# Performance work log

Hardware: AMD Instinct MI355X
Metric: run time of the kernel (lower is better)

## Reference

```python
import jax, jax.numpy as jnp
import numpy as np

B, T, N, H, L, K, E, KSEL = 16, 24, 2000, 64, 2, 2, 3, 2
OUT_LEN = 24
NUM_MAT = 1 + 2 * K  # identity + K powers of each of the 2 supports


def _rw(adj):
    # random-walk matrix D^{-1} A
    d = adj.sum(axis=1)
    return adj / jnp.where(d == 0, 1.0, d)[:, None]


def _dconv(xh, A_q, A_h, W, b):
    # k-hop dual-direction diffusion convolution; xh: [b,n,f]
    feats = [xh]
    for A in (A_q, A_h):
        cur = xh
        for _ in range(K):
            cur = jnp.einsum('nm,bmf->bnf', A, cur)
            feats.append(cur)
    return jnp.concatenate(feats, axis=-1) @ W + b


def _cell(x, h, A_q, A_h, Wg, bg, Wc, bc):
    # DCRNN (diffusion-conv GRU) cell
    xh = jnp.concatenate([x, h], axis=-1)
    ru = jax.nn.sigmoid(_dconv(xh, A_q, A_h, Wg, bg))
    r, u = jnp.split(ru, 2, axis=-1)
    c = jnp.tanh(_dconv(jnp.concatenate([x, r * h], axis=-1), A_q, A_h, Wc, bc))
    return u * h + (1.0 - u) * c


def setup_inputs() -> dict:
    key = jax.random.key(0)
    ks = jax.random.split(key, 24)
    s = 0.02
    nrm = lambda k, shp: (jax.random.normal(k, shp) * s).astype(jnp.float32)
    adj = (jax.random.uniform(ks[0], (N, N)) * (jax.random.uniform(ks[1], (N, N)) < 0.05)).astype(jnp.float32)
    x_enc = jax.random.normal(ks[2], (B, T, N, 1), dtype=jnp.float32)
    x_enc = x_enc * (jax.random.uniform(ks[3], (B, T, N, 1)) < 0.7)
    x_dec = jax.random.normal(ks[4], (B, OUT_LEN, N, 1), dtype=jnp.float32)

    def cell_p(k, fin):
        k1, k2 = jax.random.split(k)
        fcat = NUM_MAT * (fin + H)
        return (nrm(k1, (fcat, 2 * H)), jnp.zeros(2 * H, jnp.float32),
                nrm(k2, (fcat, H)), jnp.zeros(H, jnp.float32))

    e0 = cell_p(ks[5], 1)
    e1 = cell_p(ks[6], H)
    d0 = cell_p(ks[7], 1)
    d1 = cell_p(ks[8], H)
    return dict(
        adj=adj, x_enc=x_enc, x_dec=x_dec,
        gate_w1=nrm(ks[9], (T, H)), gate_b1=jnp.zeros(H, jnp.float32),
        gate_w2=nrm(ks[10], (H, E)), gate_b2=jnp.zeros(E, jnp.float32),
        ew_mean=nrm(ks[11], (T, T)), eb_mean=jnp.zeros(T, jnp.float32),
        ew_wmean=nrm(ks[12], (T, T)), eb_wmean=jnp.zeros(T, jnp.float32),
        ew_diff=nrm(ks[13], (T, T)), eb_diff=jnp.zeros(T, jnp.float32),
        enc0_Wg=e0[0], enc0_bg=e0[1], enc0_Wc=e0[2], enc0_bc=e0[3],
        enc1_Wg=e1[0], enc1_bg=e1[1], enc1_Wc=e1[2], enc1_bc=e1[3],
        dec0_Wg=d0[0], dec0_bg=d0[1], dec0_Wc=d0[2], dec0_bc=d0[3],
        dec1_Wg=d1[0], dec1_bg=d1[1], dec1_Wc=d1[2], dec1_bc=d1[3],
        fc_w=nrm(ks[14], (H, 1)), fc_b=jnp.zeros(1, jnp.float32),
        epoch=10,
    )


def reference(adj, x_enc, x_dec, gate_w1, gate_b1, gate_w2, gate_b2,
              ew_mean, eb_mean, ew_wmean, eb_wmean, ew_diff, eb_diff,
              enc0_Wg, enc0_bg, enc0_Wc, enc0_bc, enc1_Wg, enc1_bg, enc1_Wc, enc1_bc,
              dec0_Wg, dec0_bg, dec0_Wc, dec0_bc, dec1_Wg, dec1_bg, dec1_Wc, dec1_bc,
              fc_w, fc_b, epoch):
    A_q = _rw(adj)
    A_h = _rw(adj.T)

    # ---- DataPreparation: MoE-gated graph imputation ----
    x = jnp.transpose(x_enc[..., 0], (0, 2, 1))  # [b, n, t]
    g = jax.nn.relu(x @ gate_w1 + gate_b1)
    logits = g @ gate_w2 + gate_b2               # [b, n, E]
    top, idx = jax.lax.top_k(logits, KSEL)
    w = jax.nn.softmax(top, axis=-1)
    gate = (w[..., None] * jax.nn.one_hot(idx, E, dtype=x.dtype)).sum(axis=-2)  # [b,n,E]

    adj_ns = adj * (1.0 - jnp.eye(N, dtype=adj.dtype))
    deg_bin = (adj_ns > 0).astype(x.dtype)
    A_mean = deg_bin / jnp.maximum(deg_bin.sum(axis=1, keepdims=True), 1.0)
    rs = adj_ns.sum(axis=1, keepdims=True)
    A_wmean = adj_ns / jnp.where(rs == 0, 1.0, rs)
    A_diff = _rw(adj_ns)

    outs = [jnp.einsum('nm,bmt->bnt', A_agg, x) @ W + b
            for A_agg, W, b in ((A_mean, ew_mean, eb_mean),
                                (A_wmean, ew_wmean, eb_wmean),
                                (A_diff, ew_diff, eb_diff))]
    combined = (gate[..., None] * jnp.stack(outs, axis=2)).sum(axis=2)  # [b,n,t]
    x = jnp.where(x == 0, combined, x)
    x_imp = jnp.transpose(x, (0, 2, 1))[..., None]  # [b,t,n,1]

    # ---- Encoder: scan over time, 2 DCRNN layers ----
    enc_params = ((enc0_Wg, enc0_bg, enc0_Wc, enc0_bc),
                  (enc1_Wg, enc1_bg, enc1_Wc, enc1_bc))

    def enc_step(h, xt):
        inp = xt
        hs = []
        for l in range(L):
            nh = _cell(inp, h[l], A_q, A_h, *enc_params[l])
            inp = nh
            hs.append(nh)
        return jnp.stack(hs), None

    h0 = jnp.zeros((L, B, N, H), x_imp.dtype)
    hT, _ = jax.lax.scan(enc_step, h0, jnp.transpose(x_imp, (1, 0, 2, 3)))

    dec_params = ((dec0_Wg, dec0_bg, dec0_Wc, dec0_bc),
                  (dec1_Wg, dec1_bg, dec1_Wc, dec1_bc))

    def dec_step(carry, _):
        inp, h = carry
        hs = []
        for l in range(L):
            nh = _cell(inp, h[l], A_q, A_h, *dec_params[l])
            inp = nh
            hs.append(nh)
        out = nh @ fc_w + fc_b  # [b,n,1]
        return (out, jnp.stack(hs)), out

    _, outs_t = jax.lax.scan(dec_step, (x_imp[:, -1], hT), None, length=OUT_LEN)
    return jnp.transpose(outs_t, (1, 0, 2, 3))  # [b, out_len, n, 1]
```

## Files before the change

### kernel.cpp

```cpp
#include <hip/hip_runtime.h>

#define NROW 2000
#define NB   16
#define NT   24
#define NH   64
#define NM   (NROW*NB)
#define HOPLDS (NROW*64)
#define ENT_CAP 262144

typedef _Float16 h16;
typedef __attribute__((ext_vector_type(2))) _Float16 h16x2;
typedef __attribute__((ext_vector_type(8))) _Float16 h16x8;
typedef __attribute__((ext_vector_type(4))) float    f32x4;

__device__ __forceinline__ h16x2 bc_h2(unsigned int u){ union{unsigned int u; h16x2 h;} c; c.u=u; return c.h; }

__global__ __launch_bounds__(256) void k_count(const float* adj, int* cnt_q, int* cnt_h, int* cnt_ns,
    float* rsum_q, float* rsum_h, float* rsum_ns, int* deg_ns){
  int wid = (blockIdx.x*256 + threadIdx.x)>>6;
  int lane = threadIdx.x & 63;
  int kind = wid / NROW, n = wid - kind*NROW;
  int cnt = 0; float sum = 0.f;
  for (int c = lane; c < NROW; c += 64){
    float v = (kind==1) ? adj[(size_t)c*NROW + n] : adj[(size_t)n*NROW + c];
    if (kind==2 && c==n) v = 0.f;
    cnt += (v != 0.f); sum += v;
  }
  for (int off=32; off; off>>=1){ cnt += __shfl_down(cnt,off); sum += __shfl_down(sum,off); }
  if (lane==0){
    int pc = (cnt+7)&~7;
    if (kind==0){ cnt_q[n]=pc; rsum_q[n]=sum; }
    else if (kind==1){ cnt_h[n]=pc; rsum_h[n]=sum; }
    else { cnt_ns[n]=pc; rsum_ns[n]=sum; deg_ns[n]=cnt; }
  }
}

__global__ __launch_bounds__(1024) void k_scan(const int* cq, const int* ch, const int* cn,
    int* rq, int* rh, int* rn){
  __shared__ int s0[2048], s1[2048], s2[2048];
  int t = threadIdx.x;
  for (int a=0;a<2;a++){ int i=t+a*1024; s0[i]= i<NROW?cq[i]:0; s1[i]= i<NROW?ch[i]:0; s2[i]= i<NROW?cn[i]:0; }
  __syncthreads();
  for (int off=1; off<2048; off<<=1){
    int v0[2],v1[2],v2[2];
    for (int a=0;a<2;a++){ int i=t+a*1024; v0[a]= i>=off? s0[i-off]:0; v1[a]= i>=off? s1[i-off]:0; v2[a]= i>=off? s2[i-off]:0; }
    __syncthreads();
    for (int a=0;a<2;a++){ int i=t+a*1024; s0[i]+=v0[a]; s1[i]+=v1[a]; s2[i]+=v2[a]; }
    __syncthreads();
  }
  for (int a=0;a<2;a++){ int i=t+a*1024; if (i<=NROW){ rq[i]= i? s0[i-1]:0; rh[i]= i? s1[i-1]:0; rn[i]= i? s2[i-1]:0; } }
}

__global__ __launch_bounds__(1024) void k_sort(const int* c0, const int* c1, const int* c2,
                                               int* o0, int* o1, int* o2){
  const int* cnt = blockIdx.x==0 ? c0 : blockIdx.x==1 ? c1 : c2;
  int* order     = blockIdx.x==0 ? o0 : blockIdx.x==1 ? o1 : o2;
  __shared__ int hist[256];
  __shared__ int offs[256];
  int tid = threadIdx.x;
  if (tid < 256) hist[tid] = 0;
  __syncthreads();
  for (int r = tid; r < NROW; r += 1024){
    int b = cnt[r] >> 4; if (b > 255) b = 255;
    atomicAdd(&hist[b], 1);
  }
  __syncthreads();
  if (tid == 0){ int s = 0; for (int i=0;i<256;i++){ offs[i] = s; s += hist[i]; } }
  __syncthreads();
  for (int r = tid; r < NROW; r += 1024){
    int b = cnt[r] >> 4; if (b > 255) b = 255;
    int p = atomicAdd(&offs[b], 1);
    order[p] = r;
  }
}

__device__ __forceinline__ uint2 mk_ent(int c, float a){
  h16 h = (h16)a;
  unsigned short us = __builtin_bit_cast(unsigned short, h);
  return make_uint2((unsigned int)(c*64), (unsigned int)us * 0x10001u);
}

__global__ __launch_bounds__(256) void k_fill(const float* adj, const int* rptr_q, const int* rptr_h, const int* rptr_ns,
    const float* rsum_q, const float* rsum_h, const float* rsum_ns, const int* deg_ns,
    uint2* ent_q, uint2* ent_h, uint2* ent_m, uint2* ent_w){
  int wid = (blockIdx.x*256 + threadIdx.x)>>6;
  int lane = threadIdx.x & 63;
  int kind = wid / NROW, n = wid - kind*NROW;
  const int* rp = (kind==0)?rptr_q:(kind==1)?rptr_h:rptr_ns;
  int p = rp[n], pend = rp[n+1];
  float inv, invm = 0.f;
  if (kind==0){ float d = rsum_q[n]; inv = d!=0.f?1.f/d:0.f; }
  else if (kind==1){ float d = rsum_h[n]; inv = d!=0.f?1.f/d:0.f; }
  else { float d = rsum_ns[n]; inv = d!=0.f?1.f/d:0.f; int dg = deg_ns[n]; invm = 1.f/(float)(dg>1?dg:1); }
  int base = 0;
  unsigned long long below = (1ull<<lane)-1ull;
  for (int c0=0; c0<NROW; c0+=64){
    int c = c0+lane; float v = 0.f;
    if (c < NROW){ v = (kind==1)? adj[(size_t)c*NROW+n] : adj[(size_t)n*NROW+c]; if (kind==2 && c==n) v = 0.f; }
    unsigned long long m = __ballot(v != 0.f);
    if (v != 0.f){
      int pos = p + base + __popcll(m & below);
      if (kind==2){ ent_w[pos] = mk_ent(c, v*inv); ent_m[pos] = mk_ent(c, invm); }
      else if (kind==0) ent_q[pos] = mk_ent(c, v*inv);
      else              ent_h[pos] = mk_ent(c, v*inv);
    }
    base += __popcll(m);
  }
  for (int i = p+base+lane; i < pend; i += 64){
    uint2 z = make_uint2(0u,0u);
    if (kind==2){ ent_w[i]=z; ent_m[i]=z; } else if (kind==0) ent_q[i]=z; else ent_h[i]=z;
  }
}

struct HopJob { const h16* X; const int* rptr; const uint2* ent; const int* order; h16* out; };

__device__ __forceinline__ void proc2(const char* xs, int cl, uint4 p, h16x2 ha[4]){
  union{f32x4 v; h16x2 h[4];} ca, cb;
  ca.v = *(const f32x4*)(xs + p.x + cl);
  cb.v = *(const f32x4*)(xs + p.z + cl);
  h16x2 va = bc_h2(p.y), vb = bc_h2(p.w);
  ha[0] = ca.h[0]*va + ha[0];
  ha[1] = ca.h[1]*va + ha[1];
  ha[2] = ca.h[2]*va + ha[2];
  ha[3] = ca.h[3]*va + ha[3];
  ha[0] = cb.h[0]*vb + ha[0];
  ha[1] = cb.h[1]*vb + ha[1];
  ha[2] = cb.h[2]*vb + ha[2];
  ha[3] = cb.h[3]*vb + ha[3];
}

__global__ __launch_bounds__(1024) void k_hop(HopJob j0, HopJob j1, HopJob j2, HopJob j3,
                                              int coltiles, int rsplit, int C){
  extern __shared__ char xs[];
  int per = coltiles*rsplit;
  int bid = blockIdx.x;
  int jb = bid/per, rem = bid - jb*per;
  int ct = rem/rsplit, rs = rem - ct*rsplit;
  HopJob j = (jb==0)?j0:(jb==1)?j1:(jb==2)?j2:j3;
  int c0 = ct*32;
  int tid = threadIdx.x;
  {
    int r0 = tid>>2, so = tid&3;
    const char* src = (const char*)j.X + (size_t)2*(c0 + so*8);
    char* dst = xs + so*16;
    for (int r = r0; r < NROW; r += 256)
      *(f32x4*)(dst + r*64) = *(const f32x4*)(src + (size_t)2*r*C);
  }
  __syncthreads();
  int lane = tid&63, wv = tid>>6;
  int g = lane>>2;
  int cl = (lane&3)*16;
  for (int k = wv; ; k += 16){
    int gu = rs + k*rsplit;
    if (gu >= 125) break;
    int n = j.order[gu*16 + g];
    {
      int p0 = j.rptr[n], cnt = j.rptr[n+1]-p0;
      const uint4* ep4 = (const uint4*)(j.ent + p0);
      float f[8] = {0.f,0.f,0.f,0.f,0.f,0.f,0.f,0.f};
      if (cnt > 0){
        uint4 cur[8];
        #pragma unroll
        for (int u2=0;u2<8;u2++) cur[u2] = ep4[u2];
        int i = 0;
        for (; i+16 <= cnt; i += 16){
          uint4 nx[8];
          int b = (i>>1)+8;
          #pragma unroll
          for (int u2=0;u2<8;u2++) nx[u2] = ep4[b+u2];
          h16x2 ha[4] = {{(_Float16)0.f,(_Float16)0.f},{(_Float16)0.f,(_Float16)0.f},
                         {(_Float16)0.f,(_Float16)0.f},{(_Float16)0.f,(_Float16)0.f}};
          #pragma unroll
          for (int u2=0;u2<8;u2++) proc2(xs, cl, cur[u2], ha);
          f[0] += (float)ha[0][0]; f[1] += (float)ha[0][1];
          f[2] += (float)ha[1][0]; f[3] += (float)ha[1][1];
          f[4] += (float)ha[2][0]; f[5] += (float)ha[2][1];
          f[6] += (float)ha[3][0]; f[7] += (float)ha[3][1];
          #pragma unroll
          for (int u2=0;u2<8;u2++) cur[u2] = nx[u2];
        }
        if (i < cnt){
          h16x2 ha[4] = {{(_Float16)0.f,(_Float16)0.f},{(_Float16)0.f,(_Float16)0.f},
                         {(_Float16)0.f,(_Float16)0.f},{(_Float16)0.f,(_Float16)0.f}};
          proc2(xs, cl, cur[0], ha);
          proc2(xs, cl, cur[1], ha);
          proc2(xs, cl, cur[2], ha);
          proc2(xs, cl, cur[3], ha);
          f[0] += (float)ha[0][0]; f[1] += (float)ha[0][1];
          f[2] += (float)ha[1][0]; f[3] += (float)ha[1][1];
          f[4] += (float)ha[2][0]; f[5] += (float)ha[2][1];
          f[6] += (float)ha[3][0]; f[7] += (float)ha[3][1];
        }
      }
      alignas(16) h16 ov[8];
      #pragma unroll
      for (int k2=0;k2<8;k2++) ov[k2] = (h16)f[k2];
      *(uint4*)((char*)j.out + (size_t)2*((size_t)n*C + c0) + cl) = *(const uint4*)ov;
    }
  }
}

__global__ void k_evinit(const float* rq, const float* rh, float* eq, float* eh){
  int n = blockIdx.x*256+threadIdx.x; if (n>=NROW) return;
  eq[n] = rq[n]!=0.f?1.f:0.f; eh[n] = rh[n]!=0.f?1.f:0.f;
}

__global__ __launch_bounds__(256) void k_matvec(const int* rptr, const uint2* ent, const float* vin, float* vout){
  int wid = (blockIdx.x*256+threadIdx.x)>>6; int lane = threadIdx.x&63;
  if (wid >= NROW) return;
  int p0 = rptr[wid], p1 = rptr[wid+1];
  float s = 0.f;
  for (int i=p0+lane; i<p1; i+=64){
    uint2 e = ent[i];
    int idx = (int)(e.x>>6);
    h16 hv = __builtin_bit_cast(h16, (unsigned short)(e.y & 0xffffu));
    s += (float)hv * vin[idx];
  }
  for (int off=32; off; off>>=1) s += __shfl_down(s,off);
  if (lane==0) vout[wid] = s;
}

__global__ void k_bias2(const float* W, const float* fcb, const float* e1, const float* e2,
                        const float* e3, const float* e4, float* dst, int O){
  int idx = blockIdx.x*256+threadIdx.x; if (idx >= NROW*O) return;
  int n = idx/O, o = idx - n*O;
  float v = W[o] + e1[n]*W[(size_t)65*O+o] + e2[n]*W[(size_t)130*O+o]
                 + e3[n]*W[(size_t)195*O+o] + e4[n]*W[(size_t)260*O+o];
  dst[idx] = fcb[0]*v;
}

__global__ void k_wpack(const float* W, const float* fcw, h16* dst, int O, int nch, int mode){
  int idx = blockIdx.x*256+threadIdx.x; if (idx >= nch*O*32) return;
  int k = idx&31; int o = (idx>>5)%O; int ch = idx/(O*32);
  float v = 0.f;
  if (mode==0){
    if (ch < 10){ int m = ch>>1, j = (ch&1)*32 + k; v = W[(size_t)(m*65+1+j)*O + o]; }
    else if (k < 5) v = W[(size_t)(k*65)*O + o];
  } else if (mode==1){
    int m = ch>>2, j = (ch&3)*32 + k; v = W[(size_t)(m*128+j)*O + o];
  } else {
    if (ch < 10){ int m = ch>>1, j = (ch&1)*32 + k; v = fcw[j]*W[(size_t)(m*65)*O + o]; }
    else { int c2 = ch-10; int m = c2>>1, j = (c2&1)*32 + k; v = W[(size_t)(m*65+1+j)*O + o]; }
  }
  dst[(size_t)(ch*O + o)*32 + k] = (h16)v;
}

__global__ __launch_bounds__(256) void k_impute_gate(const float* x_enc, const float* gw1, const float* gb1,
// ... 181 lines not shown
{
  const float* adj   = (const float*)d_in[0];
  const float* x_enc = (const float*)d_in[1];
  const float* gw1   = (const float*)d_in[3];
  const float* gb1   = (const float*)d_in[4];
  const float* gw2   = (const float*)d_in[5];
  const float* gb2   = (const float*)d_in[6];
  const float* ewm   = (const float*)d_in[7];
  const float* ebm   = (const float*)d_in[8];
  const float* eww   = (const float*)d_in[9];
  const float* ebw   = (const float*)d_in[10];
  const float* ewd   = (const float*)d_in[11];
  const float* ebd   = (const float*)d_in[12];
  const float* Wg[4] = {(const float*)d_in[13],(const float*)d_in[17],(const float*)d_in[21],(const float*)d_in[25]};
  const float* bg[4] = {(const float*)d_in[14],(const float*)d_in[18],(const float*)d_in[22],(const float*)d_in[26]};
  const float* Wc[4] = {(const float*)d_in[15],(const float*)d_in[19],(const float*)d_in[23],(const float*)d_in[27]};
  const float* bc[4] = {(const float*)d_in[16],(const float*)d_in[20],(const float*)d_in[24],(const float*)d_in[28]};
  const float* fcw   = (const float*)d_in[29];
  const float* fcb   = (const float*)d_in[30];
  float* outp = (float*)d_out;
  (void)in_sizes; (void)n_in; (void)out_size; (void)ws_size;

  char* base = (char*)d_ws;
  size_t off = 0;
  auto alloc = [&](size_t sz)->char*{ char* p = base + off; off += (sz + 255) & ~(size_t)255; return p; };

  uint2* ent_q = (uint2*)alloc(ENT_CAP*8);
  uint2* ent_h = (uint2*)alloc(ENT_CAP*8);
  uint2* ent_m = (uint2*)alloc(ENT_CAP*8);
  uint2* ent_w = (uint2*)alloc(ENT_CAP*8);
  int* rptr_q = (int*)alloc(2001*4);
  int* rptr_h = (int*)alloc(2001*4);
  int* rptr_n = (int*)alloc(2001*4);
  int* cnt_q = (int*)alloc(NROW*4);
  int* cnt_h = (int*)alloc(NROW*4);
  int* cnt_n = (int*)alloc(NROW*4);
  int* ord_q = (int*)alloc(NROW*4);
  int* ord_h = (int*)alloc(NROW*4);
  int* ord_n = (int*)alloc(NROW*4);
  float* rsum_q = (float*)alloc(NROW*4);
  float* rsum_h = (float*)alloc(NROW*4);
  float* rsum_n = (float*)alloc(NROW*4);
  int* deg_n = (int*)alloc(NROW*4);
  float* evq1 = (float*)alloc(NROW*4);
  float* evq2 = (float*)alloc(NROW*4);
  float* evh1 = (float*)alloc(NROW*4);
  float* evh2 = (float*)alloc(NROW*4);
  float* gate3 = (float*)alloc((size_t)NM*3*4);
  h16* xpack = (h16*)alloc((size_t)NT*NM*8*2);
  h16* wp_e0g = (h16*)alloc(11*128*64); h16* wp_e0c = (h16*)alloc(11*64*64);
  h16* wp_e1g = (h16*)alloc(20*128*64); h16* wp_e1c = (h16*)alloc(20*64*64);
  h16* wp_d0gE= (h16*)alloc(11*128*64); h16* wp_d0cE= (h16*)alloc(11*64*64);
  h16* wp_d0gW= (h16*)alloc(20*128*64); h16* wp_d0cW= (h16*)alloc(20*64*64);
  h16* wp_d1g = (h16*)alloc(20*128*64); h16* wp_d1c = (h16*)alloc(20*64*64);
  float* bias2g = (float*)alloc((size_t)NROW*128*4);
  float* bias2c = (float*)alloc((size_t)NROW*64*4);
  const size_t SEG = (size_t)NM*NH*2;
  h16* h0 = (h16*)alloc(SEG);
  h16* h1 = (h16*)alloc(SEG);
  float* ub = (float*)alloc((size_t)NM*NH*4);
  h16* rh = (h16*)alloc(SEG);
  h16* zb = (h16*)alloc(SEG);
  h16* H0Q1=(h16*)alloc(SEG); h16* H0Q2=(h16*)alloc(SEG); h16* H0H1=(h16*)alloc(SEG); h16* H0H2=(h16*)alloc(SEG);
  h16* H1Q1=(h16*)alloc(SEG); h16* H1Q2=(h16*)alloc(SEG); h16* H1H1=(h16*)alloc(SEG); h16* H1H2=(h16*)alloc(SEG);
  h16* RHQ1=(h16*)alloc(SEG); h16* RHQ2=(h16*)alloc(SEG); h16* RHH1=(h16*)alloc(SEG); h16* RHH2=(h16*)alloc(SEG);
  h16* xT   = RHQ1;  h16* Zm = RHQ2;  h16* Zw = RHH1;  h16* ximp = RHH2;
  h16* xq1  = H1Q1;  h16* xq2 = H1Q2; h16* xh1 = H1H1; h16* xh2 = H1H2;

  hipFuncSetAttribute(reinterpret_cast<const void*>(k_hop),
                      hipFuncAttributeMaxDynamicSharedMemorySize, HOPLDS);

  hipMemsetAsync(zb, 0, SEG, stream);
  hipMemsetAsync(h0, 0, SEG, stream);
  hipMemsetAsync(h1, 0, SEG, stream);

  k_count<<<1500,256,0,stream>>>(adj, cnt_q, cnt_h, cnt_n, rsum_q, rsum_h, rsum_n, deg_n);
  k_sort<<<3,1024,0,stream>>>(cnt_q, cnt_h, cnt_n, ord_q, ord_h, ord_n);
  k_scan<<<1,1024,0,stream>>>(cnt_q, cnt_h, cnt_n, rptr_q, rptr_h, rptr_n);
  k_fill<<<1500,256,0,stream>>>(adj, rptr_q, rptr_h, rptr_n, rsum_q, rsum_h, rsum_n, deg_n,
                                ent_q, ent_h, ent_m, ent_w);
  k_evinit<<<8,256,0,stream>>>(rsum_q, rsum_h, evq1, evh1);
  k_matvec<<<500,256,0,stream>>>(rptr_q, ent_q, evq1, evq2);
  k_matvec<<<500,256,0,stream>>>(rptr_h, ent_h, evh1, evh2);
  k_bias2<<<1000,256,0,stream>>>(Wg[2], fcb, evq1, evq2, evh1, evh2, bias2g, 128);
  k_bias2<<<500,256,0,stream>>>(Wc[2], fcb, evq1, evq2, evh1, evh2, bias2c, 64);
  auto wpk = [&](const float* W, h16* dst, int O, int nch, int mode){
    k_wpack<<<(nch*O*32+255)/256,256,0,stream>>>(W, fcw, dst, O, nch, mode);
  };
  wpk(Wg[0], wp_e0g, 128, 11, 0); wpk(Wc[0], wp_e0c, 64, 11, 0);
  wpk(Wg[1], wp_e1g, 128, 20, 1); wpk(Wc[1], wp_e1c, 64, 20, 1);
  wpk(Wg[2], wp_d0gE,128, 11, 0); wpk(Wc[2], wp_d0cE,64, 11, 0);
  wpk(Wg[2], wp_d0gW,128, 20, 2); wpk(Wc[2], wp_d0cW,64, 20, 2);
  wpk(Wg[3], wp_d1g, 128, 20, 1); wpk(Wc[3], wp_d1c, 64, 20, 1);

  k_impute_gate<<<125,256,0,stream>>>(x_enc, gw1, gb1, gw2, gb2, gate3, xT);

  auto hop = [&](HopJob a, HopJob b, HopJob c, HopJob d, int nj, int C, int rsplit){
    int ct = C/32;
    k_hop<<<nj*ct*rsplit, 1024, HOPLDS, stream>>>(a,b,c,d, ct, rsplit, C);
  };
  HopJob JA{xT, rptr_n, ent_m, ord_n, Zm}, JB{xT, rptr_n, ent_w, ord_n, Zw};
  hop(JA, JB, JA, JB, 2, NB*NT, 10);
  k_impute_combine<<<125,256,0,stream>>>(x_enc, Zm, Zw, gate3, ewm, ebm, eww, ebw, ewd, ebd, ximp);
  HopJob X1{ximp, rptr_q, ent_q, ord_q, xq1}, X2{ximp, rptr_h, ent_h, ord_h, xh1};
  hop(X1, X2, X1, X2, 2, NB*NT, 10);
  HopJob X3{xq1, rptr_q, ent_q, ord_q, xq2}, X4{xh1, rptr_h, ent_h, ord_h, xh2};
  hop(X3, X4, X3, X4, 2, NB*NT, 10);
  k_xpack8<<<(NT*NM+255)/256,256,0,stream>>>(ximp, xq1, xq2, xh1, xh2, xpack);

  h16* HSEG0[5] = {h0, H0Q1, H0Q2, H0H1, H0H2};
  h16* HSEG1[5] = {h1, H1Q1, H1Q2, H1H1, H1H2};
  h16* RSEG[5]  = {rh, RHQ1, RHQ2, RHH1, RHH2};
  h16* ZSEG[5]  = {zb, zb, zb, zb, zb};

  auto shapeA = [&](GArgs& A, h16* const* seg, const h16* xpk){
    for (int m=0;m<5;m++) for (int s=0;s<2;s++){ int ch=2*m+s; A.src[ch]=seg[m]; A.rstrideB[ch]=NH*2; A.coffB[ch]=s*64; }
    A.src[10]=xpk; A.rstrideB[10]=16; A.coffB[10]=0; A.nchunks=11; A.xchunk=10;
  };
  auto shapeB = [&](GArgs& A, h16* const* sa, h16* const* sb){
    for (int m=0;m<5;m++) for (int s=0;s<4;s++){ int ch=4*m+s;
      A.src[ch] = (s<2)? sa[m] : sb[m]; A.rstrideB[ch]=NH*2; A.coffB[ch]=(s&1)*64; }
    A.nchunks=20; A.xchunk=-1;
  };
  auto shapeC = [&](GArgs& A, h16* const* segH, h16* const* segX){
    for (int m=0;m<5;m++) for (int s=0;s<2;s++){
      int ch=2*m+s; A.src[ch]=segX[m]; A.rstrideB[ch]=NH*2; A.coffB[ch]=s*64;
      int c2=10+2*m+s; A.src[c2]=segH[m]; A.rstrideB[c2]=NH*2; A.coffB[c2]=s*64; }
    A.nchunks=20; A.xchunk=-1;
  };
  auto common = [&](GArgs& A, const h16* wp, const float* bias, const h16* hb, const float* b2, int t){
    A.wpack=wp; A.bias=bias; A.hbuf=hb; A.rhbuf=rh; A.ubuf=ub; A.hout=(h16*)hb;
    A.bias2=b2; A.fcw=fcw; A.fcb=fcb; A.dout=outp; A.tstep=t;
  };

  for (int phase=0; phase<2; phase++){
    int ig = phase? 2 : 0;
    const h16* wpg0E = phase? wp_d0gE : wp_e0g;
    const h16* wpc0E = phase? wp_d0cE : wp_e0c;
    const h16* wpg1  = phase? wp_d1g  : wp_e1g;
    const h16* wpc1  = phase? wp_d1c  : wp_e1c;
    for (int t=0;t<NT;t++){
      bool wprime = (phase==1 && t>0);
      if (wprime){
        HopJob a{h1, rptr_q, ent_q, ord_q, H1Q1}, b{h1, rptr_h, ent_h, ord_h, H1H1};
        hop(a,b,a,b, 2, NB*NH, 4);
        HopJob c{H1Q1, rptr_q, ent_q, ord_q, H1Q2}, d{H1H1, rptr_h, ent_h, ord_h, H1H2};
        hop(c,d,c,d, 2, NB*NH, 4);
      }
      {
        GArgs A{};
        if (wprime) shapeC(A, HSEG0, HSEG1);
        else shapeA(A, (phase==0 && t==0)? ZSEG : HSEG0, xpack + (size_t)((phase==0)? t : 23)*NM*8);
        common(A, wprime? wp_d0gW : wpg0E, bg[ig], h0, bias2g, t);
        if (wprime) k_g<128,1,1,0><<<500,256,0,stream>>>(A);
        else        k_g<128,1,0,0><<<500,256,0,stream>>>(A);
      }
      if (wprime){
        HopJob a{rh, rptr_q, ent_q, ord_q, RHQ1}, b{rh, rptr_h, ent_h, ord_h, RHH1};
        hop(a,b,a,b, 2, NB*NH, 4);
        HopJob c{RHQ1, rptr_q, ent_q, ord_q, RHQ2}, d{RHH1, rptr_h, ent_h, ord_h, RHH2};
        hop(c,d,c,d, 2, NB*NH, 4);
      } else {
        HopJob a{rh, rptr_q, ent_q, ord_q, RHQ1}, b{rh, rptr_h, ent_h, ord_h, RHH1};
        HopJob c{h1, rptr_q, ent_q, ord_q, H1Q1}, d{h1, rptr_h, ent_h, ord_h, H1H1};
        hop(a,b,c,d, 4, NB*NH, 2);
        HopJob a2{RHQ1, rptr_q, ent_q, ord_q, RHQ2}, b2{RHH1, rptr_h, ent_h, ord_h, RHH2};
        HopJob c2{H1Q1, rptr_q, ent_q, ord_q, H1Q2}, d2{H1H1, rptr_h, ent_h, ord_h, H1H2};
        hop(a2,b2,c2,d2, 4, NB*NH, 2);
      }
      {
        GArgs A{};
        if (wprime) shapeC(A, RSEG, HSEG1);
        else shapeA(A, RSEG, xpack + (size_t)((phase==0)? t : 23)*NM*8);
        common(A, wprime? wp_d0cW : wpc0E, bc[ig], h0, bias2c, t);
        if (wprime) k_g<64,0,1,0><<<500,256,0,stream>>>(A);
        else        k_g<64,0,0,0><<<500,256,0,stream>>>(A);
      }
      {
        HopJob a{h0, rptr_q, ent_q, ord_q, H0Q1}, b{h0, rptr_h, ent_h, ord_h, H0H1};
        hop(a,b,a,b, 2, NB*NH, 4);
        HopJob c{H0Q1, rptr_q, ent_q, ord_q, H0Q2}, d{H0H1, rptr_h, ent_h, ord_h, H0H2};
        hop(c,d,c,d, 2, NB*NH, 4);
      }
      {
        GArgs A{};
        shapeB(A, HSEG0, HSEG1);
        common(A, wpg1, bg[ig+1], h1, nullptr, t);
        k_g<128,1,0,0><<<500,256,0,stream>>>(A);
      }
      {
        HopJob a{rh, rptr_q, ent_q, ord_q, RHQ1}, b{rh, rptr_h, ent_h, ord_h, RHH1};
        hop(a,b,a,b, 2, NB*NH, 4);
        HopJob c{RHQ1, rptr_q, ent_q, ord_q, RHQ2}, d{RHH1, rptr_h, ent_h, ord_h, RHH2};
        hop(c,d,c,d, 2, NB*NH, 4);
      }
      {
        GArgs A{};
        shapeB(A, HSEG0, RSEG);
        common(A, wpc1, bc[ig+1], h1, nullptr, t);
        if (phase) k_g<64,0,0,1><<<500,256,0,stream>>>(A);
        else       k_g<64,0,0,0><<<500,256,0,stream>>>(A);
      }
    }
  }
}
```

Measured before the change: 13.03 ms.

## Split sparse hop into two row-halves with 64-column LDS tiles

Each CSR row is split into two segments by column (<1000 and >=1000), padded separately, with a new rmid array. The hop kernel now stages only 1000 rows of X at a time but 64 columns wide (128B per row) in LDS. It accumulates the first half, restages the second half, and accumulates again, with each wave processing 4 output rows held in registers. The aim is to halve the number of column tiles per job (so less redundant entry reading across tiles) and widen each gather. The cost is a second sync-and-stage pass, extra padding, and a shorter unroll per chunk. Rsplit values are raised to keep enough blocks in flight.

```diff
diff --git a/kernel.cpp b/kernel.cpp
--- a/kernel.cpp
+++ b/kernel.cpp
@@ -5,7 +5,7 @@
 #define NT   24
 #define NH   64
 #define NM   (NROW*NB)
-#define HOPLDS (NROW*64)
+#define HOPLDS (1000*128)
 #define ENT_CAP 262144
 
 typedef _Float16 h16;
@@ -15,23 +15,26 @@
 
 __device__ __forceinline__ h16x2 bc_h2(unsigned int u){ union{unsigned int u; h16x2 h;} c; c.u=u; return c.h; }
 
-__global__ __launch_bounds__(256) void k_count(const float* adj, int* cnt_q, int* cnt_h, int* cnt_ns,
-    float* rsum_q, float* rsum_h, float* rsum_ns, int* deg_ns){
+__global__ __launch_bounds__(256) void k_count(const float* adj, int* cnt_q, int* cnt_h, int* cnt_n,
+    int* pA_q, int* pA_h, int* pA_n,
+    float* rsum_q, float* rsum_h, float* rsum_n, int* deg_n){
   int wid = (blockIdx.x*256 + threadIdx.x)>>6;
   int lane = threadIdx.x & 63;
   int kind = wid / NROW, n = wid - kind*NROW;
-  int cnt = 0; float sum = 0.f;
+  int cA = 0, cB = 0; float sum = 0.f;
   for (int c = lane; c < NROW; c += 64){
     float v = (kind==1) ? adj[(size_t)c*NROW + n] : adj[(size_t)n*NROW + c];
     if (kind==2 && c==n) v = 0.f;
-    cnt += (v != 0.f); sum += v;
-  }
-  for (int off=32; off; off>>=1){ cnt += __shfl_down(cnt,off); sum += __shfl_down(sum,off); }
+    if (v != 0.f){ if (c < 1000) cA++; else cB++; sum += v; }
+  }
+  for (int off=32; off; off>>=1){
+    cA += __shfl_down(cA,off); cB += __shfl_down(cB,off); sum += __shfl_down(sum,off);
+  }
   if (lane==0){
-    int pc = (cnt+7)&~7;
-    if (kind==0){ cnt_q[n]=pc; rsum_q[n]=sum; }
-    else if (kind==1){ cnt_h[n]=pc; rsum_h[n]=sum; }
-    else { cnt_ns[n]=pc; rsum_ns[n]=sum; deg_ns[n]=cnt; }
+    int pa = (cA+7)&~7, pb = (cB+7)&~7;
+    if (kind==0){ cnt_q[n]=pa+pb; pA_q[n]=pa; rsum_q[n]=sum; }
+    else if (kind==1){ cnt_h[n]=pa+pb; pA_h[n]=pa; rsum_h[n]=sum; }
+    else { cnt_n[n]=pa+pb; pA_n[n]=pa; rsum_n[n]=sum; deg_n[n]=cA+cB; }
   }
 }
 
@@ -51,6 +54,16 @@
   for (int a=0;a<2;a++){ int i=t+a*1024; if (i<=NROW){ rq[i]= i? s0[i-1]:0; rh[i]= i? s1[i-1]:0; rn[i]= i? s2[i-1]:0; } }
 }
 
+__global__ void k_rmid(const int* rq, const int* rh, const int* rn,
+                       const int* paq, const int* pah, const int* pan,
+                       int* mq, int* mh, int* mn){
+  int i = blockIdx.x*256+threadIdx.x; if (i >= 3*NROW) return;
+  int kind = i/NROW, n = i - kind*NROW;
+  if (kind==0) mq[n] = rq[n]+paq[n];
+  else if (kind==1) mh[n] = rh[n]+pah[n];
+  else mn[n] = rn[n]+pan[n];
+}
+
 __global__ __launch_bounds__(1024) void k_sort(const int* c0, const int* c1, const int* c2,
                                                int* o0, int* o1, int* o2){
   const int* cnt = blockIdx.x==0 ? c0 : blockIdx.x==1 ? c1 : c2;
@@ -74,45 +87,55 @@
   }
 }
 
-__device__ __forceinline__ uint2 mk_ent(int c, float a){
+__device__ __forceinline__ uint2 mk_ent(unsigned int off_bytes, float a){
   h16 h = (h16)a;
   unsigned short us = __builtin_bit_cast(unsigned short, h);
-  return make_uint2((unsigned int)(c*64), (unsigned int)us * 0x10001u);
-}
-
-__global__ __launch_bounds__(256) void k_fill(const float* adj, const int* rptr_q, const int* rptr_h, const int* rptr_ns,
-    const float* rsum_q, const float* rsum_h, const float* rsum_ns, const int* deg_ns,
+  return make_uint2(off_bytes, (unsigned int)us * 0x10001u);
+}
+
+__global__ __launch_bounds__(256) void k_fill(const float* adj,
+    const int* rptr_q, const int* rptr_h, const int* rptr_n,
+    const int* rmid_q, const int* rmid_h, const int* rmid_n,
+    const float* rsum_q, const float* rsum_h, const float* rsum_n, const int* deg_n,
     uint2* ent_q, uint2* ent_h, uint2* ent_m, uint2* ent_w){
   int wid = (blockIdx.x*256 + threadIdx.x)>>6;
   int lane = threadIdx.x & 63;
   int kind = wid / NROW, n = wid - kind*NROW;
-  const int* rp = (kind==0)?rptr_q:(kind==1)?rptr_h:rptr_ns;
-  int p = rp[n], pend = rp[n+1];
+  const int* rp = (kind==0)?rptr_q:(kind==1)?rptr_h:rptr_n;
+  const int* rm = (kind==0)?rmid_q:(kind==1)?rmid_h:rmid_n;
+  int p = rp[n], pend = rp[n+1], mid = rm[n];
   float inv, invm = 0.f;
   if (kind==0){ float d = rsum_q[n]; inv = d!=0.f?1.f/d:0.f; }
   else if (kind==1){ float d = rsum_h[n]; inv = d!=0.f?1.f/d:0.f; }
-  else { float d = rsum_ns[n]; inv = d!=0.f?1.f/d:0.f; int dg = deg_ns[n]; invm = 1.f/(float)(dg>1?dg:1); }
-  int base = 0;
+  else { float d = rsum_n[n]; inv = d!=0.f?1.f/d:0.f; int dg = deg_n[n]; invm = 1.f/(float)(dg>1?dg:1); }
+  int baseA = 0, baseB = 0;
   unsigned long long below = (1ull<<lane)-1ull;
   for (int c0=0; c0<NROW; c0+=64){
     int c = c0+lane; float v = 0.f;
     if (c < NROW){ v = (kind==1)? adj[(size_t)c*NROW+n] : adj[(size_t)n*NROW+c]; if (kind==2 && c==n) v = 0.f; }
-    unsigned long long m = __ballot(v != 0.f);
-    if (v != 0.f){
-      int pos = p + base + __popcll(m & below);
-      if (kind==2){ ent_w[pos] = mk_ent(c, v*inv); ent_m[pos] = mk_ent(c, invm); }
-      else if (kind==0) ent_q[pos] = mk_ent(c, v*inv);
-      else              ent_h[pos] = mk_ent(c, v*inv);
-    }
-    base += __popcll(m);
-  }
-  for (int i = p+base+lane; i < pend; i += 64){
-    uint2 z = make_uint2(0u,0u);
+    bool nz = (v != 0.f);
+    unsigned long long mA = __ballot(nz && c < 1000);
+    unsigned long long mB = __ballot(nz && c >= 1000);
+    if (nz){
+      int pos; unsigned int off;
+      if (c < 1000){ pos = p + baseA + __popcll(mA & below); off = (unsigned int)(c*128); }
+      else         { pos = mid + baseB + __popcll(mB & below); off = (unsigned int)((c-1000)*128); }
+      if (kind==2){ ent_w[pos] = mk_ent(off, v*inv); ent_m[pos] = mk_ent(off, invm); }
+      else if (kind==0) ent_q[pos] = mk_ent(off, v*inv);
+      else              ent_h[pos] = mk_ent(off, v*inv);
+    }
+    baseA += __popcll(mA); baseB += __popcll(mB);
+  }
+  uint2 z = make_uint2(0u,0u);
+  for (int i = p+baseA+lane; i < mid; i += 64){
     if (kind==2){ ent_w[i]=z; ent_m[i]=z; } else if (kind==0) ent_q[i]=z; else ent_h[i]=z;
   }
-}
-
-struct HopJob { const h16* X; const int* rptr; const uint2* ent; const int* order; h16* out; };
+  for (int i = mid+baseB+lane; i < pend; i += 64){
+    if (kind==2){ ent_w[i]=z; ent_m[i]=z; } else if (kind==0) ent_q[i]=z; else ent_h[i]=z;
+  }
+}
+
+struct HopJob { const h16* X; const int* rptr; const int* rmid; const uint2* ent; const int* order; h16* out; };
 
 __device__ __forceinline__ void proc2(const char* xs, int cl, uint4 p, h16x2 ha[4]){
   union{f32x4 v; h16x2 h[4];} ca, cb;
@@ -129,6 +152,34 @@
   ha[3] = cb.h[3]*vb + ha[3];
 }
 
+__device__ __forceinline__ void accum_row(const char* xs, int cl, const uint2* ent,
+                                          int p0, int p1, float f[8]){
+  int cnt = p1 - p0;
+  if (cnt <= 0) return;
+  const uint4* ep4 = (const uint4*)(ent + p0);
+  uint4 cur[4];
+  #pragma unroll
+  for (int u=0;u<4;u++) cur[u] = ep4[u];
+  for (int i=0; i<cnt; i+=8){
+    uint4 nx[4];
+    if (i+8 < cnt){
+      int b = (i>>1)+4;
+      #pragma unroll
+      for (int u=0;u<4;u++) nx[u] = ep4[b+u];
+    }
+    h16x2 ha[4] = {{(_Float16)0.f,(_Float16)0.f},{(_Float16)0.f,(_Float16)0.f},
+                   {(_Float16)0.f,(_Float16)0.f},{(_Float16)0.f,(_Float16)0.f}};
+    #pragma unroll
+    for (int u=0;u<4;u++) proc2(xs, cl, cur[u], ha);
+    f[0] += (float)ha[0][0]; f[1] += (float)ha[0][1];
+    f[2] += (float)ha[1][0]; f[3] += (float)ha[1][1];
+    f[4] += (float)ha[2][0]; f[5] += (float)ha[2][1];
+    f[6] += (float)ha[3][0]; f[7] += (float)ha[3][1];
+    #pragma unroll
+    for (int u=0;u<4;u++) cur[u] = nx[u];
+  }
+}
+
 __global__ __launch_bounds__(1024) void k_hop(HopJob j0, HopJob j1, HopJob j2, HopJob j3,
                                               int coltiles, int rsplit, int C){
   extern __shared__ char xs[];
@@ -137,64 +188,54 @@
   int jb = bid/per, rem = bid - jb*per;
   int ct = rem/rsplit, rs = rem - ct*rsplit;
   HopJob j = (jb==0)?j0:(jb==1)?j1:(jb==2)?j2:j3;
-  int c0 = ct*32;
+  int c0 = ct*64;
   int tid = threadIdx.x;
+  int lane = tid&63, wv = tid>>6;
+  int g = lane>>3;
+  int cl = (lane&7)*16;
+
+  int nslot[4];
+  #pragma unroll
+  for (int u=0;u<4;u++){
+    int gu = rs + (wv + u*16)*rsplit;
+    nslot[u] = (gu < 250) ? j.order[gu*8 + g] : -1;
+  }
+  float f[4][8];
+  #pragma unroll
+  for (int u=0;u<4;u++)
+    #pragma unroll
+    for (int k2=0;k2<8;k2++) f[u][k2] = 0.f;
+
   {
-    int r0 = tid>>2, so = tid&3;
+    int r0 = tid>>3, so = tid&7;
     const char* src = (const char*)j.X + (size_t)2*(c0 + so*8);
     char* dst = xs + so*16;
-    for (int r = r0; r < NROW; r += 256)
-      *(f32x4*)(dst + r*64) = *(const f32x4*)(src + (size_t)2*r*C);
+    for (int r = r0; r < 1000; r += 128)
+      *(f32x4*)(dst + r*128) = *(const f32x4*)(src + (size_t)2*(size_t)r*C);
   }
   __syncthreads();
-  int lane = tid&63, wv = tid>>6;
-  int g = lane>>2;
-  int cl = (lane&3)*16;
-  for (int k = wv; ; k += 16){
-    int gu = rs + k*rsplit;
-    if (gu >= 125) break;
-    int n = j.order[gu*16 + g];
-    {
-      int p0 = j.rptr[n], cnt = j.rptr[n+1]-p0;
-      const uint4* ep4 = (const uint4*)(j.ent + p0);
-      float f[8] = {0.f,0.f,0.f,0.f,0.f,0.f,0.f,0.f};
-      if (cnt > 0){
-        uint4 cur[8];
-        #pragma unroll
-        for (int u2=0;u2<8;u2++) cur[u2] = ep4[u2];
-        int i = 0;
-        for (; i+16 <= cnt; i += 16){
-          uint4 nx[8];
-          int b = (i>>1)+8;
-          #pragma unroll
-          for (int u2=0;u2<8;u2++) nx[u2] = ep4[b+u2];
-          h16x2 ha[4] = {{(_Float16)0.f,(_Float16)0.f},{(_Float16)0.f,(_Float16)0.f},
-                         {(_Float16)0.f,(_Float16)0.f},{(_Float16)0.f,(_Float16)0.f}};
-          #pragma unroll
-          for (int u2=0;u2<8;u2++) proc2(xs, cl, cur[u2], ha);
-          f[0] += (float)ha[0][0]; f[1] += (float)ha[0][1];
-          f[2] += (float)ha[1][0]; f[3] += (float)ha[1][1];
-          f[4] += (float)ha[2][0]; f[5] += (float)ha[2][1];
-          f[6] += (float)ha[3][0]; f[7] += (float)ha[3][1];
-          #pragma unroll
-          for (int u2=0;u2<8;u2++) cur[u2] = nx[u2];
-        }
-        if (i < cnt){
-          h16x2 ha[4] = {{(_Float16)0.f,(_Float16)0.f},{(_Float16)0.f,(_Float16)0.f},
-                         {(_Float16)0.f,(_Float16)0.f},{(_Float16)0.f,(_Float16)0.f}};
-          proc2(xs, cl, cur[0], ha);
-          proc2(xs, cl, cur[1], ha);
-          proc2(xs, cl, cur[2], ha);
-          proc2(xs, cl, cur[3], ha);
-          f[0] += (float)ha[0][0]; f[1] += (float)ha[0][1];
-          f[2] += (float)ha[1][0]; f[3] += (float)ha[1][1];
-          f[4] += (float)ha[2][0]; f[5] += (float)ha[2][1];
-          f[6] += (float)ha[3][0]; f[7] += (float)ha[3][1];
-        }
-      }
+  #pragma unroll
+  for (int u=0;u<4;u++){
+    int n = nslot[u];
+    if (n >= 0) accum_row(xs, cl, j.ent, j.rptr[n], j.rmid[n], f[u]);
+  }
+  __syncthreads();
+  {
+    int r0 = tid>>3, so = tid&7;
+    const char* src = (const char*)j.X + (size_t)2*((size_t)1000*C + c0 + so*8);
+    char* dst = xs + so*16;
+    for (int r = r0; r < 1000; r += 128)
+      *(f32x4*)(dst + r*128) = *(const f32x4*)(src + (size_t)2*(size_t)r*C);
+  }
+  __syncthreads();
+  #pragma unroll
+  for (int u=0;u<4;u++){
+    int n = nslot[u];
+    if (n >= 0){
+      accum_row(xs, cl, j.ent, j.rmid[n], j.rptr[n+1], f[u]);
       alignas(16) h16 ov[8];
       #pragma unroll
-      for (int k2=0;k2<8;k2++) ov[k2] = (h16)f[k2];
+      for (int k2=0;k2<8;k2++) ov[k2] = (h16)f[u][k2];
       *(uint4*)((char*)j.out + (size_t)2*((size_t)n*C + c0) + cl) = *(const uint4*)ov;
     }
   }
@@ -205,14 +246,15 @@
   eq[n] = rq[n]!=0.f?1.f:0.f; eh[n] = rh[n]!=0.f?1.f:0.f;
 }
 
-__global__ __launch_bounds__(256) void k_matvec(const int* rptr, const uint2* ent, const float* vin, float* vout){
+__global__ __launch_bounds__(256) void k_matvec(const int* rptr, const int* rmid, const uint2* ent,
+                                                const float* vin, float* vout){
   int wid = (blockIdx.x*256+threadIdx.x)>>6; int lane = threadIdx.x&63;
   if (wid >= NROW) return;
-  int p0 = rptr[wid], p1 = rptr[wid+1];
+  int p0 = rptr[wid], p1 = rptr[wid+1], mid = rmid[wid];
   float s = 0.f;
   for (int i=p0+lane; i<p1; i+=64){
     uint2 e = ent[i];
-    int idx = (int)(e.x>>6);
+    int idx = (int)(e.x>>7) + ((i >= mid) ? 1000 : 0);
     h16 hv = __builtin_bit_cast(h16, (unsigned short)(e.y & 0xffffu));
     s += (float)hv * vin[idx];
   }
@@ -460,9 +502,15 @@
   int* rptr_q = (int*)alloc(2001*4);
   int* rptr_h = (int*)alloc(2001*4);
   int* rptr_n = (int*)alloc(2001*4);
+  int* rmid_q = (int*)alloc(NROW*4);
+  int* rmid_h = (int*)alloc(NROW*4);
+  int* rmid_n = (int*)alloc(NROW*4);
   int* cnt_q = (int*)alloc(NROW*4);
   int* cnt_h = (int*)alloc(NROW*4);
   int* cnt_n = (int*)alloc(NROW*4);
+  int* pA_q = (int*)alloc(NROW*4);
+  int* pA_h = (int*)alloc(NROW*4);
+  int* pA_n = (int*)alloc(NROW*4);
   int* ord_q = (int*)alloc(NROW*4);
   int* ord_h = (int*)alloc(NROW*4);
   int* ord_n = (int*)alloc(NROW*4);
@@ -502,14 +550,17 @@
   hipMemsetAsync(h0, 0, SEG, stream);
   hipMemsetAsync(h1, 0, SEG, stream);
 
-  k_count<<<1500,256,0,stream>>>(adj, cnt_q, cnt_h, cnt_n, rsum_q, rsum_h, rsum_n, deg_n);
+  k_count<<<1500,256,0,stream>>>(adj, cnt_q, cnt_h, cnt_n, pA_q, pA_h, pA_n,
+                                 rsum_q, rsum_h, rsum_n, deg_n);
   k_sort<<<3,1024,0,stream>>>(cnt_q, cnt_h, cnt_n, ord_q, ord_h, ord_n);
   k_scan<<<1,1024,0,stream>>>(cnt_q, cnt_h, cnt_n, rptr_q, rptr_h, rptr_n);
-  k_fill<<<1500,256,0,stream>>>(adj, rptr_q, rptr_h, rptr_n, rsum_q, rsum_h, rsum_n, deg_n,
+  k_rmid<<<24,256,0,stream>>>(rptr_q, rptr_h, rptr_n, pA_q, pA_h, pA_n, rmid_q, rmid_h, rmid_n);
+  k_fill<<<1500,256,0,stream>>>(adj, rptr_q, rptr_h, rptr_n, rmid_q, rmid_h, rmid_n,
+                                rsum_q, rsum_h, rsum_n, deg_n,
                                 ent_q, ent_h, ent_m, ent_w);
   k_evinit<<<8,256,0,stream>>>(rsum_q, rsum_h, evq1, evh1);
-  k_matvec<<<500,256,0,stream>>>(rptr_q, ent_q, evq1, evq2);
-  k_matvec<<<500,256,0,stream>>>(rptr_h, ent_h, evh1, evh2);
+  k_matvec<<<500,256,0,stream>>>(rptr_q, rmid_q, ent_q, evq1, evq2);
+  k_matvec<<<500,256,0,stream>>>(rptr_h, rmid_h, ent_h, evh1, evh2);
   k_bias2<<<1000,256,0,stream>>>(Wg[2], fcb, evq1, evq2, evh1, evh2, bias2g, 128);
   k_bias2<<<500,256,0,stream>>>(Wc[2], fcb, evq1, evq2, evh1, evh2, bias2c, 64);
   auto wpk = [&](const float* W, h16* dst, int O, int nch, int mode){
@@ -524,16 +575,16 @@
   k_impute_gate<<<125,256,0,stream>>>(x_enc, gw1, gb1, gw2, gb2, gate3, xT);
 
   auto hop = [&](HopJob a, HopJob b, HopJob c, HopJob d, int nj, int C, int rsplit){
-    int ct = C/32;
+    int ct = C/64;
     k_hop<<<nj*ct*rsplit, 1024, HOPLDS, stream>>>(a,b,c,d, ct, rsplit, C);
   };
-  HopJob JA{xT, rptr_n, ent_m, ord_n, Zm}, JB{xT, rptr_n, ent_w, ord_n, Zw};
-  hop(JA, JB, JA, JB, 2, NB*NT, 10);
+  HopJob JA{xT, rptr_n, rmid_n, ent_m, ord_n, Zm}, JB{xT, rptr_n, rmid_n, ent_w, ord_n, Zw};
+  hop(JA, JB, JA, JB, 2, NB*NT, 16);
   k_impute_combine<<<125,256,0,stream>>>(x_enc, Zm, Zw, gate3, ewm, ebm, eww, ebw, ewd, ebd, ximp);
-  HopJob X1{ximp, rptr_q, ent_q, ord_q, xq1}, X2{ximp, rptr_h, ent_h, ord_h, xh1};
-  hop(X1, X2, X1, X2, 2, NB*NT, 10);
-  HopJob X3{xq1, rptr_q, ent_q, ord_q, xq2}, X4{xh1, rptr_h, ent_h, ord_h, xh2};
-  hop(X3, X4, X3, X4, 2, NB*NT, 10);
+  HopJob X1{ximp, rptr_q, rmid_q, ent_q, ord_q, xq1}, X2{ximp, rptr_h, rmid_h, ent_h, ord_h, xh1};
+  hop(X1, X2, X1, X2, 2, NB*NT, 16);
+  HopJob X3{xq1, rptr_q, rmid_q, ent_q, ord_q, xq2}, X4{xh1, rptr_h, rmid_h, ent_h, ord_h, xh2};
+  hop(X3, X4, X3, X4, 2, NB*NT, 16);
   k_xpack8<<<(NT*NM+255)/256,256,0,stream>>>(ximp, xq1, xq2, xh1, xh2, xpack);
 
   h16* HSEG0[5] = {h0, H0Q1, H0Q2, H0H1, H0H2};
@@ -570,10 +621,10 @@
     for (int t=0;t<NT;t++){
       bool wprime = (phase==1 && t>0);
       if (wprime){
-        HopJob a{h1, rptr_q, ent_q, ord_q, H1Q1}, b{h1, rptr_h, ent_h, ord_h, H1H1};
-        hop(a,b,a,b, 2, NB*NH, 4);
-        HopJob c{H1Q1, rptr_q, ent_q, ord_q, H1Q2}, d{H1H1, rptr_h, ent_h, ord_h, H1H2};
-        hop(c,d,c,d, 2, NB*NH, 4);
+        HopJob a{h1, rptr_q, rmid_q, ent_q, ord_q, H1Q1}, b{h1, rptr_h, rmid_h, ent_h, ord_h, H1H1};
+        hop(a,b,a,b, 2, NB*NH, 8);
+        HopJob c{H1Q1, rptr_q, rmid_q, ent_q, ord_q, H1Q2}, d{H1H1, rptr_h, rmid_h, ent_h, ord_h, H1H2};
+        hop(c,d,c,d, 2, NB*NH, 8);
       }
       {
         GArgs A{};
@@ -584,17 +635,17 @@
         else        k_g<128,1,0,0><<<500,256,0,stream>>>(A);
       }
       if (wprime){
-        HopJob a{rh, rptr_q, ent_q, ord_q, RHQ1}, b{rh, rptr_h, ent_h, ord_h, RHH1};
-        hop(a,b,a,b, 2, NB*NH, 4);
-        HopJob c{RHQ1, rptr_q, ent_q, ord_q, RHQ2}, d{RHH1, rptr_h, ent_h, ord_h, RHH2};
-        hop(c,d,c,d, 2, NB*NH, 4);
+        HopJob a{rh, rptr_q, rmid_q, ent_q, ord_q, RHQ1}, b{rh, rptr_h, rmid_h, ent_h, ord_h, RHH1};
+        hop(a,b,a,b, 2, NB*NH, 8);
+        HopJob c{RHQ1, rptr_q, rmid_q, ent_q, ord_q, RHQ2}, d{RHH1, rptr_h, rmid_h, ent_h, ord_h, RHH2};
+        hop(c,d,c,d, 2, NB*NH, 8);
       } else {
-        HopJob a{rh, rptr_q, ent_q, ord_q, RHQ1}, b{rh, rptr_h, ent_h, ord_h, RHH1};
-        HopJob c{h1, rptr_q, ent_q, ord_q, H1Q1}, d{h1, rptr_h, ent_h, ord_h, H1H1};
-        hop(a,b,c,d, 4, NB*NH, 2);
-        HopJob a2{RHQ1, rptr_q, ent_q, ord_q, RHQ2}, b2{RHH1, rptr_h, ent_h, ord_h, RHH2};
-        HopJob c2{H1Q1, rptr_q, ent_q, ord_q, H1Q2}, d2{H1H1, rptr_h, ent_h, ord_h, H1H2};
-        hop(a2,b2,c2,d2, 4, NB*NH, 2);
+        HopJob a{rh, rptr_q, rmid_q, ent_q, ord_q, RHQ1}, b{rh, rptr_h, rmid_h, ent_h, ord_h, RHH1};
+        HopJob c{h1, rptr_q, rmid_q, ent_q, ord_q, H1Q1}, d{h1, rptr_h, rmid_h, ent_h, ord_h, H1H1};
+        hop(a,b,c,d, 4, NB*NH, 4);
+        HopJob a2{RHQ1, rptr_q, rmid_q, ent_q, ord_q, RHQ2}, b2{RHH1, rptr_h, rmid_h, ent_h, ord_h, RHH2};
+        HopJob c2{H1Q1, rptr_q, rmid_q, ent_q, ord_q, H1Q2}, d2{H1H1, rptr_h, rmid_h, ent_h, ord_h, H1H2};
+        hop(a2,b2,c2,d2, 4, NB*NH, 4);
       }
       {
         GArgs A{};
@@ -605,10 +656,10 @@
         else        k_g<64,0,0,0><<<500,256,0,stream>>>(A);
       }
       {
-        HopJob a{h0, rptr_q, ent_q, ord_q, H0Q1}, b{h0, rptr_h, ent_h, ord_h, H0H1};
-        hop(a,b,a,b, 2, NB*NH, 4);
-        HopJob c{H0Q1, rptr_q, ent_q, ord_q, H0Q2}, d{H0H1, rptr_h, ent_h, ord_h, H0H2};
-        hop(c,d,c,d, 2, NB*NH, 4);
+        HopJob a{h0, rptr_q, rmid_q, ent_q, ord_q, H0Q1}, b{h0, rptr_h, rmid_h, ent_h, ord_h, H0H1};
+        hop(a,b,a,b, 2, NB*NH, 8);
+        HopJob c{H0Q1, rptr_q, rmid_q, ent_q, ord_q, H0Q2}, d{H0H1, rptr_h, rmid_h, ent_h, ord_h, H0H2};
+        hop(c,d,c,d, 2, NB*NH, 8);
       }
       {
         GArgs A{};
@@ -617,10 +668,10 @@
         k_g<128,1,0,0><<<500,256,0,stream>>>(A);
       }
       {
-        HopJob a{rh, rptr_q, ent_q, ord_q, RHQ1}, b{rh, rptr_h, ent_h, ord_h, RHH1};
-        hop(a,b,a,b, 2, NB*NH, 4);
-        HopJob c{RHQ1, rptr_q, ent_q, ord_q, RHQ2}, d{RHH1, rptr_h, ent_h, ord_h, RHH2};
-        hop(c,d,c,d, 2, NB*NH, 4);
+        HopJob a{rh, rptr_q, rmid_q, ent_q, ord_q, RHQ1}, b{rh, rptr_h, rmid_h, ent_h, ord_h, RHH1};
+        hop(a,b,a,b, 2, NB*NH, 8);
+        HopJob c{RHQ1, rptr_q, rmid_q, ent_q, ord_q, RHQ2}, d{RHH1, rptr_h, rmid_h, ent_h, ord_h, RHH2};
+        hop(c,d,c,d, 2, NB*NH, 8);
       }
       {
         GArgs A{};
```

Measured after the change: 16.02 ms. 22.9% more time.

## Fuse consecutive diffusion hops into one persistent kernel with grid barrier

Applied to the files above, without the earlier changes.

Merges each pair of dependent sparse hop launches (hop 1 then hop 2) into a single 256-block kernel that synchronizes via an atomic software grid barrier, removing a kernel launch and tail drain per pair. Also guards the entry prefetch so it does not read past a row's list. Relies on all 256 blocks being co-resident (one per CU); if that fails the barrier deadlocks. The barrier counter is never reset but uses generation counting.

```diff
diff --git a/kernel.cpp b/kernel.cpp
--- a/kernel.cpp
+++ b/kernel.cpp
@@ -129,14 +129,7 @@
   ha[3] = cb.h[3]*vb + ha[3];
 }
 
-__global__ __launch_bounds__(1024) void k_hop(HopJob j0, HopJob j1, HopJob j2, HopJob j3,
-                                              int coltiles, int rsplit, int C){
-  extern __shared__ char xs[];
-  int per = coltiles*rsplit;
-  int bid = blockIdx.x;
-  int jb = bid/per, rem = bid - jb*per;
-  int ct = rem/rsplit, rs = rem - ct*rsplit;
-  HopJob j = (jb==0)?j0:(jb==1)?j1:(jb==2)?j2:j3;
+__device__ void hop_body(HopJob j, int ct, int rs, int rsplit, int C, char* xs){
   int c0 = ct*32;
   int tid = threadIdx.x;
   {
@@ -165,9 +158,11 @@
         int i = 0;
         for (; i+16 <= cnt; i += 16){
           uint4 nx[8];
-          int b = (i>>1)+8;
-          #pragma unroll
-          for (int u2=0;u2<8;u2++) nx[u2] = ep4[b+u2];
+          if (i+16 < cnt){
+            int b = (i>>1)+8;
+            #pragma unroll
+            for (int u2=0;u2<8;u2++) nx[u2] = ep4[b+u2];
+          }
           h16x2 ha[4] = {{(_Float16)0.f,(_Float16)0.f},{(_Float16)0.f,(_Float16)0.f},
                          {(_Float16)0.f,(_Float16)0.f},{(_Float16)0.f,(_Float16)0.f}};
           #pragma unroll
@@ -197,6 +192,53 @@
       for (int k2=0;k2<8;k2++) ov[k2] = (h16)f[k2];
       *(uint4*)((char*)j.out + (size_t)2*((size_t)n*C + c0) + cl) = *(const uint4*)ov;
     }
+  }
+}
+
+__global__ __launch_bounds__(1024) void k_hop(HopJob j0, HopJob j1, HopJob j2, HopJob j3,
+                                              int coltiles, int rsplit, int C){
+  extern __shared__ char xs[];
+  int per = coltiles*rsplit;
+  int bid = blockIdx.x;
+  int jb = bid/per, rem = bid - jb*per;
+  int ct = rem/rsplit, rs = rem - ct*rsplit;
+  HopJob j = (jb==0)?j0:(jb==1)?j1:(jb==2)?j2:j3;
+  hop_body(j, ct, rs, rsplit, C, xs);
+}
+
+__device__ __forceinline__ void grid_barrier(unsigned* bar, unsigned nblk){
+  __syncthreads();
+  if (threadIdx.x == 0){
+    __threadfence();
+    unsigned my = atomicAdd(&bar[0], 1u);
+    unsigned gen = my / nblk;
+    if ((my % nblk) == nblk - 1u) atomicAdd(&bar[1], 1u);
+    while (atomicAdd(&bar[1], 0u) <= gen) __builtin_amdgcn_s_sleep(8);
+    __threadfence();
+  }
+  __syncthreads();
+}
+
+struct Hop2Args {
+  HopJob a0, a1, a2, a3;
+  HopJob b0, b1, b2, b3;
+  int per, rsplit, C;
+  unsigned* bar;
+};
+
+__global__ __launch_bounds__(1024) void k_hop2(Hop2Args A){
+  extern __shared__ char xs[];
+  int bid = blockIdx.x;
+  int jb = bid/A.per, rem = bid - jb*A.per;
+  int ct = rem/A.rsplit, rs = rem - ct*A.rsplit;
+  {
+    HopJob j = (jb==0)?A.a0:(jb==1)?A.a1:(jb==2)?A.a2:A.a3;
+    hop_body(j, ct, rs, A.rsplit, A.C, xs);
+  }
+  grid_barrier(A.bar, 256u);
+  {
+    HopJob j = (jb==0)?A.b0:(jb==1)?A.b1:(jb==2)?A.b2:A.b3;
+    hop_body(j, ct, rs, A.rsplit, A.C, xs);
   }
 }
 
@@ -474,6 +516,7 @@
   float* evq2 = (float*)alloc(NROW*4);
   float* evh1 = (float*)alloc(NROW*4);
   float* evh2 = (float*)alloc(NROW*4);
+  unsigned* bar = (unsigned*)alloc(256);
   float* gate3 = (float*)alloc((size_t)NM*3*4);
   h16* xpack = (h16*)alloc((size_t)NT*NM*8*2);
   h16* wp_e0g = (h16*)alloc(11*128*64); h16* wp_e0c = (h16*)alloc(11*64*64);
@@ -497,7 +540,10 @@
 
   hipFuncSetAttribute(reinterpret_cast<const void*>(k_hop),
                       hipFuncAttributeMaxDynamicSharedMemorySize, HOPLDS);
-
+  hipFuncSetAttribute(reinterpret_cast<const void*>(k_hop2),
+                      hipFuncAttributeMaxDynamicSharedMemorySize, HOPLDS);
+
+  hipMemsetAsync(bar, 0, 8, stream);
   hipMemsetAsync(zb, 0, SEG, stream);
   hipMemsetAsync(h0, 0, SEG, stream);
   hipMemsetAsync(h1, 0, SEG, stream);
@@ -527,6 +573,15 @@
     int ct = C/32;
     k_hop<<<nj*ct*rsplit, 1024, HOPLDS, stream>>>(a,b,c,d, ct, rsplit, C);
   };
+  auto hop2 = [&](HopJob a0, HopJob a1, HopJob a2_, HopJob a3,
+                  HopJob b0, HopJob b1, HopJob b2_, HopJob b3, int C, int rsplit){
+    Hop2Args A;
+    A.a0=a0; A.a1=a1; A.a2=a2_; A.a3=a3;
+    A.b0=b0; A.b1=b1; A.b2=b2_; A.b3=b3;
+    A.per = (C/32)*rsplit; A.rsplit = rsplit; A.C = C; A.bar = bar;
+    k_hop2<<<256, 1024, HOPLDS, stream>>>(A);
+  };
+
   HopJob JA{xT, rptr_n, ent_m, ord_n, Zm}, JB{xT, rptr_n, ent_w, ord_n, Zw};
   hop(JA, JB, JA, JB, 2, NB*NT, 10);
   k_impute_combine<<<125,256,0,stream>>>(x_enc, Zm, Zw, gate3, ewm, ebm, eww, ebw, ewd, ebd, ximp);
@@ -571,9 +626,8 @@
       bool wprime = (phase==1 && t>0);
       if (wprime){
         HopJob a{h1, rptr_q, ent_q, ord_q, H1Q1}, b{h1, rptr_h, ent_h, ord_h, H1H1};
-        hop(a,b,a,b, 2, NB*NH, 4);
         HopJob c{H1Q1, rptr_q, ent_q, ord_q, H1Q2}, d{H1H1, rptr_h, ent_h, ord_h, H1H2};
-        hop(c,d,c,d, 2, NB*NH, 4);
+        hop2(a,b,a,b, c,d,c,d, NB*NH, 4);
       }
       {
         GArgs A{};
@@ -585,16 +639,14 @@
       }
       if (wprime){
         HopJob a{rh, rptr_q, ent_q, ord_q, RHQ1}, b{rh, rptr_h, ent_h, ord_h, RHH1};
-        hop(a,b,a,b, 2, NB*NH, 4);
         HopJob c{RHQ1, rptr_q, ent_q, ord_q, RHQ2}, d{RHH1, rptr_h, ent_h, ord_h, RHH2};
-        hop(c,d,c,d, 2, NB*NH, 4);
+        hop2(a,b,a,b, c,d,c,d, NB*NH, 4);
       } else {
         HopJob a{rh, rptr_q, ent_q, ord_q, RHQ1}, b{rh, rptr_h, ent_h, ord_h, RHH1};
         HopJob c{h1, rptr_q, ent_q, ord_q, H1Q1}, d{h1, rptr_h, ent_h, ord_h, H1H1};
-        hop(a,b,c,d, 4, NB*NH, 2);
         HopJob a2{RHQ1, rptr_q, ent_q, ord_q, RHQ2}, b2{RHH1, rptr_h, ent_h, ord_h, RHH2};
         HopJob c2{H1Q1, rptr_q, ent_q, ord_q, H1Q2}, d2{H1H1, rptr_h, ent_h, ord_h, H1H2};
-        hop(a2,b2,c2,d2, 4, NB*NH, 2);
+        hop2(a,b,c,d, a2,b2,c2,d2, NB*NH, 2);
       }
       {
         GArgs A{};
@@ -606,9 +658,8 @@
       }
       {
         HopJob a{h0, rptr_q, ent_q, ord_q, H0Q1}, b{h0, rptr_h, ent_h, ord_h, H0H1};
-        hop(a,b,a,b, 2, NB*NH, 4);
         HopJob c{H0Q1, rptr_q, ent_q, ord_q, H0Q2}, d{H0H1, rptr_h, ent_h, ord_h, H0H2};
-        hop(c,d,c,d, 2, NB*NH, 4);
+        hop2(a,b,a,b, c,d,c,d, NB*NH, 4);
       }
       {
         GArgs A{};
@@ -618,9 +669,8 @@
       }
       {
         HopJob a{rh, rptr_q, ent_q, ord_q, RHQ1}, b{rh, rptr_h, ent_h, ord_h, RHH1};
-        hop(a,b,a,b, 2, NB*NH, 4);
         HopJob c{RHQ1, rptr_q, ent_q, ord_q, RHQ2}, d{RHH1, rptr_h, ent_h, ord_h, RHH2};
-        hop(c,d,c,d, 2, NB*NH, 4);
+        hop2(a,b,a,b, c,d,c,d, NB*NH, 4);
       }
       {
         GArgs A{};
```

Result: slower. 16.45 ms (+26.2%).
